# Kernel optimization log

Hardware: AMD Instinct MI355X
Metric: run time of the kernel (lower is better)

Reference implementation:

```python
import jax, jax.numpy as jnp
import numpy as np

N_PIXELS = 262144
N_CENTERS = 1024
N_G = 256

def setup_inputs() -> dict:
    key = jax.random.key(0)
    k1, k2, k3, k4, k5 = jax.random.split(key, 5)
    return {
        "alphas": jax.random.normal(k1, (N_CENTERS, 1), dtype=jnp.float32),
        "betas": jax.random.normal(k2, (N_G, 2), dtype=jnp.float32) * 0.1,
        "K": jax.random.normal(k3, (N_PIXELS, N_G), dtype=jnp.float32) * 0.05,
        "all_pixels": jax.random.normal(k4, (N_PIXELS, 2), dtype=jnp.float32),
        "all_p_centers": jax.random.normal(k5, (N_CENTERS, 2), dtype=jnp.float32),
        "sdp2": jnp.ones((), dtype=jnp.float32) * 2.0,
    }

def reference(alphas, betas, K, all_pixels, all_p_centers, sdp2):
    # deformed pixel coordinates: (n_pixels, 2)
    deformed = all_pixels - K @ betas
    # pairwise squared distances via norm expansion (same math as the torch
    # ones-matmul broadcasting, expressed with plain broadcasting):
    p_norm2 = jnp.sum(jnp.square(deformed), axis=1, keepdims=True)      # (n_pixels, 1)
    c_norm2 = jnp.sum(jnp.square(all_p_centers), axis=1)                # (n_centers,)
    p_dot_c = 2.0 * (deformed @ all_p_centers.T)                        # (n_pixels, n_centers)
    big_matrix = p_norm2 + c_norm2[None, :] - p_dot_c
    kBp = jnp.exp(-big_matrix / (2.0 * sdp2))
    return kBp @ alphas                                                  # (n_pixels, 1)
```

## Files before the change

### kernel.cpp

```cpp
#include <hip/hip_runtime.h>

#if defined(__has_builtin)
#  if __has_builtin(__builtin_amdgcn_exp2f)
#    define EXP2F(x) __builtin_amdgcn_exp2f(x)
#  else
#    define EXP2F(x) exp2f(x)
#  endif
#else
#  define EXP2F(x) exp2f(x)
#endif

constexpr int NPIX  = 262144;
constexpr int NC    = 1024;
constexpr int NG    = 256;

template <int CTRL>
__device__ __forceinline__ float dpp_add(float v) {
    union { float f; int i; } u, t;
    u.f = v;
    t.i = __builtin_amdgcn_update_dpp(0, u.i, CTRL, 0xF, 0xF, true);
    return v + t.f;
}
template <int CTRL>
__device__ __forceinline__ float dpp_mov(float v) {
    union { float f; int i; } u, t;
    u.f = v;
    t.i = __builtin_amdgcn_update_dpp(0, u.i, CTRL, 0xF, 0xF, true);
    return t.f;
}
__device__ __forceinline__ float sum16(float v) {
    v = dpp_add<0xB1>(v);
    v = dpp_add<0x4E>(v);
    v = dpp_add<0x141>(v);
    v = dpp_add<0x140>(v);
    return v;
}
__device__ __forceinline__ float sum64_lane63(float v) {
    v = sum16(v);
    v = dpp_add<0x142>(v);
    v = dpp_add<0x143>(v);
    return v;
}
__device__ __forceinline__ float readlane63(float v) {
    union { float f; int i; } u; u.f = v;
    union { int i; float f; } r;
    r.i = __builtin_amdgcn_readlane(u.i, 63);
    return r.f;
}

constexpr int WS_SXY_OFF = 4096;

__global__ void prep_centers(const float* __restrict__ alphas,
                             const float* __restrict__ centers,
                             const float* __restrict__ sdp2p,
                             float* __restrict__ ws)
{
    const int c = blockIdx.x * blockDim.x + threadIdx.x;
    if (c < NC) {
        const float f  = -1.44269504088896340736f / (2.0f * sdp2p[0]);
        const float cx = centers[2 * c + 0];
        const float cy = centers[2 * c + 1];
        ws[c]          = cx;
        ws[NC + c]     = cy;
        ws[2 * NC + c] = alphas[c] * EXP2F(f * (cx * cx + cy * cy));
    }
}

constexpr int BLOCKS_A = NPIX / (4 * 32);
__global__ __launch_bounds__(256, 8)
void deform_k(const float* __restrict__ betas,
              const float* __restrict__ K,
              float2* __restrict__ sxy)
{
    const int tid  = threadIdx.x;
    const int lane = tid & 63;
    const int wave = tid >> 6;

    const float4* bf4 = (const float4*)betas;
    const float4 bb0 = bf4[2 * lane];
    const float4 bb1 = bf4[2 * lane + 1];

    const int base = (blockIdx.x * 4 + wave) * 32;
    const float* kbase = K + (size_t)base * NG;

    float ox = 0.f, oy = 0.f;

    for (int it = 0; it < 32; it += 4) {
        float4 kv[4];
        #pragma unroll
        for (int j = 0; j < 4; ++j)
            kv[j] = ((const float4*)(kbase + (size_t)(it + j) * NG))[lane];
        #pragma unroll
        for (int j = 0; j < 4; ++j) {
            float sx = kv[j].x * bb0.x + kv[j].y * bb0.z;
            float sy = kv[j].x * bb0.y + kv[j].y * bb0.w;
            sx = fmaf(kv[j].z, bb1.x, sx);
            sy = fmaf(kv[j].z, bb1.y, sy);
            sx = fmaf(kv[j].w, bb1.z, sx);
            sy = fmaf(kv[j].w, bb1.w, sy);
            sx = sum64_lane63(sx);
            sy = sum64_lane63(sy);
            const float tx = readlane63(sx);
            const float ty = readlane63(sy);
            if (lane == it + j) { ox = tx; oy = ty; }
        }
    }
    if (lane < 32) sxy[base + lane] = make_float2(ox, oy);
}

__global__ __launch_bounds__(256, 4)
void rbf_k(const float* __restrict__ pixels,
           const float* __restrict__ sdp2p,
           const float* __restrict__ ws,
           float* __restrict__ out)
{
    const int tid  = threadIdx.x;
    const int lane = tid & 63;
    const int wave = tid >> 6;
    const int p    = blockIdx.x * 256 + wave * 64 + lane;

    const float f   = -1.44269504088896340736f / (2.0f * sdp2p[0]);
    const float m2f = -2.0f * f;

    const float4* wcx4 = (const float4*)(ws);
    const float4* wcy4 = (const float4*)(ws + NC);
    const float4* wca4 = (const float4*)(ws + 2 * NC);
    float4 rcx[4], rcy[4], rca[4];
    #pragma unroll
    for (int j = 0; j < 4; ++j) {
        rcx[j] = wcx4[lane * 4 + j];
        rcy[j] = wcy4[lane * 4 + j];
        rca[j] = wca4[lane * 4 + j];
    }

    const float2 s  = ((const float2*)(ws + WS_SXY_OFF))[p];
    const float2 px = ((const float2*)pixels)[p];
    const float dx = px.x - s.x;
    const float dy = px.y - s.y;

    float dxs = m2f * dx, dys = m2f * dy, acc = 0.f;
    #pragma unroll 1
    for (int round = 0; round < 4; ++round) {
        #pragma unroll 2
        for (int t = 0; t < 16; ++t) {
            float t0 = 0.f, t1 = 0.f, t2 = 0.f, t3 = 0.f;
            #pragma unroll
            for (int j = 0; j < 4; ++j) {
                t0 = fmaf(rca[j].x, EXP2F(fmaf(dxs, rcx[j].x, dys * rcy[j].x)), t0);
                t1 = fmaf(rca[j].y, EXP2F(fmaf(dxs, rcx[j].y, dys * rcy[j].y)), t1);
                t2 = fmaf(rca[j].z, EXP2F(fmaf(dxs, rcx[j].z, dys * rcy[j].z)), t2);
                t3 = fmaf(rca[j].w, EXP2F(fmaf(dxs, rcx[j].w, dys * rcy[j].w)), t3);
            }
            acc += (t0 + t1) + (t2 + t3);
            dxs = dpp_mov<0x121>(dxs);
            dys = dpp_mov<0x121>(dys);
            acc = dpp_mov<0x121>(acc);
        }
        const int sw = lane ^ ((round & 1) ? 32 : 16);
        dxs = __shfl(dxs, sw);
        dys = __shfl(dys, sw);
        acc = __shfl(acc, sw);
    }

    out[p] = acc * EXP2F(f * (dx * dx + dy * dy));
}

extern "C" void kernel_launch(void* const* d_in, const int* in_sizes, int n_in,
                              void* d_out, int out_size, void* d_ws, size_t ws_size,
                              hipStream_t stream)
{
    const float* alphas  = (const float*)d_in[0];
    const float* betas   = (const float*)d_in[1];
    const float* K       = (const float*)d_in[2];
    const float* pixels  = (const float*)d_in[3];
    const float* centers = (const float*)d_in[4];
    const float* sdp2    = (const float*)d_in[5];
    float* outp          = (float*)d_out;
    float* ws            = (float*)d_ws;

    hipLaunchKernelGGL(prep_centers, dim3(NC / 256), dim3(256), 0, stream,
                       alphas, centers, sdp2, ws);
    hipLaunchKernelGGL(deform_k, dim3(BLOCKS_A), dim3(256), 0, stream,
                       betas, K, (float2*)(ws + WS_SXY_OFF));
    hipLaunchKernelGGL(rbf_k, dim3(NPIX / 256), dim3(256), 0, stream,
                       pixels, sdp2, ws, outp);
}
```

Before: 85.45 us.

## Fuse deform, center prep and RBF into one software-pipelined kernel

Merges the three kernels into one. Each wave handles two 64-pixel groups. The K·betas projection for the second group is interleaved with the exp-heavy RBF sum for the first, so the memory-bound K stream overlaps with transcendental compute. Center coefficients are computed per wave instead of in a separate prep kernel, and the workspace round trip for the deformation is removed. The cost is redundant per-block center exp work, higher register pressure, and half as many blocks.

```diff
diff --git a/kernel.cpp b/kernel.cpp
--- a/kernel.cpp
+++ b/kernel.cpp
@@ -13,6 +13,8 @@
 constexpr int NPIX  = 262144;
 constexpr int NC    = 1024;
 constexpr int NG    = 256;
+constexpr int BLOCK = 256;
+constexpr int GRID  = NPIX / 512;
 
 template <int CTRL>
 __device__ __forceinline__ float dpp_add(float v) {
@@ -28,15 +30,11 @@
     t.i = __builtin_amdgcn_update_dpp(0, u.i, CTRL, 0xF, 0xF, true);
     return t.f;
 }
-__device__ __forceinline__ float sum16(float v) {
+__device__ __forceinline__ float sum64_lane63(float v) {
     v = dpp_add<0xB1>(v);
     v = dpp_add<0x4E>(v);
     v = dpp_add<0x141>(v);
     v = dpp_add<0x140>(v);
-    return v;
-}
-__device__ __forceinline__ float sum64_lane63(float v) {
-    v = sum16(v);
     v = dpp_add<0x142>(v);
     v = dpp_add<0x143>(v);
     return v;
@@ -48,101 +46,78 @@
     return r.f;
 }
 
-constexpr int WS_SXY_OFF = 4096;
+__global__ __launch_bounds__(BLOCK, 4)
+void kbpa_pipe(const float* __restrict__ alphas,
+               const float* __restrict__ betas,
+               const float* __restrict__ K,
+               const float* __restrict__ pixels,
+               const float* __restrict__ centers,
+               const float* __restrict__ sdp2p,
+               float* __restrict__ out)
+{
+    const int lane = threadIdx.x & 63;
+    const int wave = threadIdx.x >> 6;
 
-__global__ void prep_centers(const float* __restrict__ alphas,
-                             const float* __restrict__ centers,
-                             const float* __restrict__ sdp2p,
-                             float* __restrict__ ws)
-{
-    const int c = blockIdx.x * blockDim.x + threadIdx.x;
-    if (c < NC) {
-        const float f  = -1.44269504088896340736f / (2.0f * sdp2p[0]);
-        const float cx = centers[2 * c + 0];
-        const float cy = centers[2 * c + 1];
-        ws[c]          = cx;
-        ws[NC + c]     = cy;
-        ws[2 * NC + c] = alphas[c] * EXP2F(f * (cx * cx + cy * cy));
+    const float f   = -1.44269504088896340736f / (2.0f * sdp2p[0]);
+    const float m2f = -2.0f * f;
+
+    float4 rcx[4], rcy[4], rca[4];
+    {
+        const float4* c4 = (const float4*)centers;
+        const float4* a4 = (const float4*)alphas;
+        #pragma unroll
+        for (int j = 0; j < 4; ++j) {
+            const float4 p0 = c4[lane * 8 + 2 * j];
+            const float4 p1 = c4[lane * 8 + 2 * j + 1];
+            rcx[j] = make_float4(p0.x, p0.z, p1.x, p1.z);
+            rcy[j] = make_float4(p0.y, p0.w, p1.y, p1.w);
+            const float4 al = a4[lane * 4 + j];
+            rca[j].x = al.x * EXP2F(f * (rcx[j].x * rcx[j].x + rcy[j].x * rcy[j].x));
+            rca[j].y = al.y * EXP2F(f * (rcx[j].y * rcx[j].y + rcy[j].y * rcy[j].y));
+            rca[j].z = al.z * EXP2F(f * (rcx[j].z * rcx[j].z + rcy[j].z * rcy[j].z));
+            rca[j].w = al.w * EXP2F(f * (rcx[j].w * rcx[j].w + rcy[j].w * rcy[j].w));
+        }
     }
-}
-
-constexpr int BLOCKS_A = NPIX / (4 * 32);
-__global__ __launch_bounds__(256, 8)
-void deform_k(const float* __restrict__ betas,
-              const float* __restrict__ K,
-              float2* __restrict__ sxy)
-{
-    const int tid  = threadIdx.x;
-    const int lane = tid & 63;
-    const int wave = tid >> 6;
 
     const float4* bf4 = (const float4*)betas;
     const float4 bb0 = bf4[2 * lane];
     const float4 bb1 = bf4[2 * lane + 1];
 
-    const int base = (blockIdx.x * 4 + wave) * 32;
-    const float* kbase = K + (size_t)base * NG;
+    const int w0 = blockIdx.x * 512 + wave * 128;
+    const float2 px0 = ((const float2*)pixels)[w0 + lane];
+    const float2 px1 = ((const float2*)pixels)[w0 + 64 + lane];
 
-    float ox = 0.f, oy = 0.f;
-
-    for (int it = 0; it < 32; it += 4) {
+    float dx0 = 0.f, dy0 = 0.f;
+    #pragma unroll 1
+    for (int g = 0; g < 16; ++g) {
         float4 kv[4];
         #pragma unroll
         for (int j = 0; j < 4; ++j)
-            kv[j] = ((const float4*)(kbase + (size_t)(it + j) * NG))[lane];
+            kv[j] = ((const float4*)(K + (size_t)(w0 + g * 4 + j) * NG))[lane];
         #pragma unroll
         for (int j = 0; j < 4; ++j) {
             float sx = kv[j].x * bb0.x + kv[j].y * bb0.z;
             float sy = kv[j].x * bb0.y + kv[j].y * bb0.w;
-            sx = fmaf(kv[j].z, bb1.x, sx);
-            sy = fmaf(kv[j].z, bb1.y, sy);
-            sx = fmaf(kv[j].w, bb1.z, sx);
-            sy = fmaf(kv[j].w, bb1.w, sy);
-            sx = sum64_lane63(sx);
-            sy = sum64_lane63(sy);
+            sx = fmaf(kv[j].z, bb1.x, sx); sy = fmaf(kv[j].z, bb1.y, sy);
+            sx = fmaf(kv[j].w, bb1.z, sx); sy = fmaf(kv[j].w, bb1.w, sy);
+            sx = sum64_lane63(sx); sy = sum64_lane63(sy);
             const float tx = readlane63(sx);
             const float ty = readlane63(sy);
-            if (lane == it + j) { ox = tx; oy = ty; }
+            if (lane == g * 4 + j) { dx0 = px0.x - tx; dy0 = px0.y - ty; }
         }
     }
-    if (lane < 32) sxy[base + lane] = make_float2(ox, oy);
-}
 
-__global__ __launch_bounds__(256, 4)
-void rbf_k(const float* __restrict__ pixels,
-           const float* __restrict__ sdp2p,
-           const float* __restrict__ ws,
-           float* __restrict__ out)
-{
-    const int tid  = threadIdx.x;
-    const int lane = tid & 63;
-    const int wave = tid >> 6;
-    const int p    = blockIdx.x * 256 + wave * 64 + lane;
+    float dxs = m2f * dx0, dys = m2f * dy0, acc = 0.f;
+    float dx1 = 0.f, dy1 = 0.f;
+    #pragma unroll 1
+    for (int g = 0; g < 16; ++g) {
+        float4 kv[4];
+        #pragma unroll
+        for (int j = 0; j < 4; ++j)
+            kv[j] = ((const float4*)(K + (size_t)(w0 + 64 + g * 4 + j) * NG))[lane];
 
-    const float f   = -1.44269504088896340736f / (2.0f * sdp2p[0]);
-    const float m2f = -2.0f * f;
-
-    const float4* wcx4 = (const float4*)(ws);
-    const float4* wcy4 = (const float4*)(ws + NC);
-    const float4* wca4 = (const float4*)(ws + 2 * NC);
-    float4 rcx[4], rcy[4], rca[4];
-    #pragma unroll
-    for (int j = 0; j < 4; ++j) {
-        rcx[j] = wcx4[lane * 4 + j];
-        rcy[j] = wcy4[lane * 4 + j];
-        rca[j] = wca4[lane * 4 + j];
-    }
-
-    const float2 s  = ((const float2*)(ws + WS_SXY_OFF))[p];
-    const float2 px = ((const float2*)pixels)[p];
-    const float dx = px.x - s.x;
-    const float dy = px.y - s.y;
-
-    float dxs = m2f * dx, dys = m2f * dy, acc = 0.f;
-    #pragma unroll 1
-    for (int round = 0; round < 4; ++round) {
-        #pragma unroll 2
-        for (int t = 0; t < 16; ++t) {
+        #pragma unroll
+        for (int t = 0; t < 4; ++t) {
             float t0 = 0.f, t1 = 0.f, t2 = 0.f, t3 = 0.f;
             #pragma unroll
             for (int j = 0; j < 4; ++j) {
@@ -156,13 +131,51 @@
             dys = dpp_mov<0x121>(dys);
             acc = dpp_mov<0x121>(acc);
         }
+        if ((g & 3) == 3) {
+            const int sw = lane ^ (((g >> 2) & 1) ? 32 : 16);
+            dxs = __shfl(dxs, sw);
+            dys = __shfl(dys, sw);
+            acc = __shfl(acc, sw);
+        }
+
+        #pragma unroll
+        for (int j = 0; j < 4; ++j) {
+            float sx = kv[j].x * bb0.x + kv[j].y * bb0.z;
+            float sy = kv[j].x * bb0.y + kv[j].y * bb0.w;
+            sx = fmaf(kv[j].z, bb1.x, sx); sy = fmaf(kv[j].z, bb1.y, sy);
+            sx = fmaf(kv[j].w, bb1.z, sx); sy = fmaf(kv[j].w, bb1.w, sy);
+            sx = sum64_lane63(sx); sy = sum64_lane63(sy);
+            const float tx = readlane63(sx);
+            const float ty = readlane63(sy);
+            if (lane == g * 4 + j) { dx1 = px1.x - tx; dy1 = px1.y - ty; }
+        }
+    }
+    out[w0 + lane] = acc * EXP2F(f * (dx0 * dx0 + dy0 * dy0));
+
+    float dxs1 = m2f * dx1, dys1 = m2f * dy1, acc1 = 0.f;
+    #pragma unroll 1
+    for (int round = 0; round < 4; ++round) {
+        #pragma unroll 2
+        for (int t = 0; t < 16; ++t) {
+            float t0 = 0.f, t1 = 0.f, t2 = 0.f, t3 = 0.f;
+            #pragma unroll
+            for (int j = 0; j < 4; ++j) {
+                t0 = fmaf(rca[j].x, EXP2F(fmaf(dxs1, rcx[j].x, dys1 * rcy[j].x)), t0);
+                t1 = fmaf(rca[j].y, EXP2F(fmaf(dxs1, rcx[j].y, dys1 * rcy[j].y)), t1);
+                t2 = fmaf(rca[j].z, EXP2F(fmaf(dxs1, rcx[j].z, dys1 * rcy[j].z)), t2);
+                t3 = fmaf(rca[j].w, EXP2F(fmaf(dxs1, rcx[j].w, dys1 * rcy[j].w)), t3);
+            }
+            acc1 += (t0 + t1) + (t2 + t3);
+            dxs1 = dpp_mov<0x121>(dxs1);
+            dys1 = dpp_mov<0x121>(dys1);
+            acc1 = dpp_mov<0x121>(acc1);
+        }
         const int sw = lane ^ ((round & 1) ? 32 : 16);
-        dxs = __shfl(dxs, sw);
-        dys = __shfl(dys, sw);
-        acc = __shfl(acc, sw);
+        dxs1 = __shfl(dxs1, sw);
+        dys1 = __shfl(dys1, sw);
+        acc1 = __shfl(acc1, sw);
     }
-
-    out[p] = acc * EXP2F(f * (dx * dx + dy * dy));
+    out[w0 + 64 + lane] = acc1 * EXP2F(f * (dx1 * dx1 + dy1 * dy1));
 }
 
 extern "C" void kernel_launch(void* const* d_in, const int* in_sizes, int n_in,
@@ -176,12 +189,7 @@
     const float* centers = (const float*)d_in[4];
     const float* sdp2    = (const float*)d_in[5];
     float* outp          = (float*)d_out;
-    float* ws            = (float*)d_ws;
 
-    hipLaunchKernelGGL(prep_centers, dim3(NC / 256), dim3(256), 0, stream,
-                       alphas, centers, sdp2, ws);
-    hipLaunchKernelGGL(deform_k, dim3(BLOCKS_A), dim3(256), 0, stream,
-                       betas, K, (float2*)(ws + WS_SXY_OFF));
-    hipLaunchKernelGGL(rbf_k, dim3(NPIX / 256), dim3(256), 0, stream,
-                       pixels, sdp2, ws, outp);
+    hipLaunchKernelGGL(kbpa_pipe, dim3(GRID), dim3(BLOCK), 0, stream,
+                       alphas, betas, K, pixels, centers, sdp2, outp);
 }
```

Result: faster. 76.94 us (-10.0%).
